# Performance work log

Measured on AMD Instinct MI355X. Metric: run time of the kernel, lower is better.

## Reference

```python
import jax, jax.numpy as jnp
import numpy as np

N_NODES = 50000
N_EDGES = 800000
IN_CH = 128
HID_CH = 128
OUT_CH = 64
K = 25
LRELU_SLOPE = 0.01  # torch.nn.LeakyReLU default
NORM_EPS = 1e-12    # F.normalize default eps


def setup_inputs() -> dict:
    key = jax.random.key(0)
    ks = jax.random.split(key, 8)
    x = jax.random.normal(ks[0], (N_NODES, IN_CH), dtype=jnp.float32)
    edge_index = jax.random.randint(ks[1], (2, N_EDGES), 0, N_NODES, dtype=jnp.int32)
    # ChebConv per-order weights [K, in, hid] + bias
    W = jax.random.normal(ks[2], (K, IN_CH, HID_CH), dtype=jnp.float32) / np.sqrt(IN_CH)
    b = jax.random.normal(ks[3], (HID_CH,), dtype=jnp.float32) * 0.01
    # mu / logstd linear heads
    w_mu = jax.random.normal(ks[4], (HID_CH, OUT_CH), dtype=jnp.float32) / np.sqrt(HID_CH)
    b_mu = jax.random.normal(ks[5], (OUT_CH,), dtype=jnp.float32) * 0.01
    w_ls = jax.random.normal(ks[6], (HID_CH, OUT_CH), dtype=jnp.float32) / np.sqrt(HID_CH)
    b_ls = jax.random.normal(ks[7], (OUT_CH,), dtype=jnp.float32) * 0.01
    return {"x": x, "edge_index": edge_index, "W": W, "b": b,
            "w_mu": w_mu, "b_mu": b_mu, "w_ls": w_ls, "b_ls": b_ls}


def _cheb_conv(x, edge_index, W, b):
    # PyG ChebConv with normalization='sym', lambda_max=2.0:
    # scaled Laplacian L~ = L - I = -D^{-1/2} A D^{-1/2} (diagonal nets to zero)
    src, dst = edge_index[0], edge_index[1]
    deg = jax.ops.segment_sum(jnp.ones(src.shape[0], x.dtype), src, num_segments=x.shape[0])
    dis = jnp.where(deg > 0, jax.lax.rsqrt(jnp.where(deg > 0, deg, 1.0)), 0.0)
    enorm = -dis[src] * dis[dst]  # [E]

    def prop(h):  # out[i] = sum_{(j->i)} enorm_e * h[j]
        return jax.ops.segment_sum(enorm[:, None] * h[src], dst, num_segments=h.shape[0])

    tx0 = x
    tx1 = prop(x)
    out0 = tx0 @ W[0] + tx1 @ W[1]

    def step(carry, Wk):
        t1, t0, acc = carry
        t2 = 2.0 * prop(t1) - t0  # Chebyshev recurrence
        return (t2, t1, acc + t2 @ Wk), None

    (_, _, out), _ = jax.lax.scan(step, (tx1, tx0, out0), W[2:])
    return out + b


def reference(x, edge_index, W, b, w_mu, b_mu, w_ls, b_ls):
    h = _cheb_conv(x, edge_index, W, b)
    # eval mode: dropout is identity
    h = jnp.where(h > 0, h, LRELU_SLOPE * h)
    mu = h @ w_mu + b_mu
    ls = h @ w_ls + b_ls
    nrm = jnp.sqrt(jnp.sum(ls * ls, axis=1, keepdims=True))
    logstd = ls / jnp.maximum(nrm, NORM_EPS) * 1.8
    zeta = mu  # eval-mode reparam returns mu
    return (mu, logstd, zeta)
```

## Files before the change

### kernel.cpp

```cpp
#include <hip/hip_runtime.h>
#include <hip/hip_fp16.h>

#define N_NODES 50000
#define N_EDGES 800000
#define CH 128
#define OUT_CH 64
#define K_ORD 25
#define SLICE ((size_t)N_NODES * CH)

typedef __attribute__((ext_vector_type(8))) short s16x8;
typedef __attribute__((ext_vector_type(4))) float f32x4;

union U4H8 { uint4 u; __half2 h2[4]; ushort us[8]; };

__global__ void count_kernel(const int* __restrict__ ei, float* __restrict__ deg,
                             int* __restrict__ indeg, int E) {
    int e = blockIdx.x * blockDim.x + threadIdx.x;
    if (e >= E) return;
    int s = ei[e];
    int d = ei[E + e];
    atomicAdd(&deg[s], 1.0f);
    atomicAdd(&indeg[d], 1);
}

__global__ __launch_bounds__(256) void scan1_kernel(const int* __restrict__ indeg,
                                                    int* __restrict__ loc,
                                                    int* __restrict__ bsum, int n) {
    __shared__ int tmp[256];
    int tid = threadIdx.x;
    int i = blockIdx.x * 256 + tid;
    int v = (i < n) ? indeg[i] : 0;
    tmp[tid] = v;
    __syncthreads();
    for (int off = 1; off < 256; off <<= 1) {
        int t = (tid >= off) ? tmp[tid - off] : 0;
        __syncthreads();
        tmp[tid] += t;
        __syncthreads();
    }
    if (i < n) loc[i] = tmp[tid] - v;
    if (tid == 255) bsum[blockIdx.x] = tmp[255];
}

__global__ __launch_bounds__(256) void scan2_kernel(int* __restrict__ bsum, int nb) {
    __shared__ int tmp[256];
    int tid = threadIdx.x;
    int v = (tid < nb) ? bsum[tid] : 0;
    tmp[tid] = v;
    __syncthreads();
    for (int off = 1; off < 256; off <<= 1) {
        int t = (tid >= off) ? tmp[tid - off] : 0;
        __syncthreads();
        tmp[tid] += t;
        __syncthreads();
    }
    if (tid < nb) bsum[tid] = tmp[tid] - v;
    if (tid == 255) bsum[nb] = tmp[255];
}

__global__ __launch_bounds__(256) void scan3_kernel(const int* __restrict__ loc,
                                                    const int* __restrict__ bsum,
                                                    int* __restrict__ rowptr,
                                                    int* __restrict__ cursor, int n, int nb) {
    int i = blockIdx.x * 256 + threadIdx.x;
    if (i < n) {
        int r = loc[i] + bsum[i >> 8];
        rowptr[i] = r;
        cursor[i] = r;
    }
    if (i == n) rowptr[n] = bsum[nb];
}

__global__ void scatter_kernel(const int* __restrict__ ei, const float* __restrict__ deg,
                               int* __restrict__ cursor, int* __restrict__ col,
                               float* __restrict__ ew, int E) {
    int e = blockIdx.x * blockDim.x + threadIdx.x;
    if (e >= E) return;
    int s = ei[e];
    int d = ei[E + e];
    float ds = deg[s], dd = deg[d];
    float dis_s = ds > 0.f ? rsqrtf(ds) : 0.f;
    float dis_d = dd > 0.f ? rsqrtf(dd) : 0.f;
    int pos = atomicAdd(&cursor[d], 1);
    col[pos] = s;
    ew[pos] = -dis_s * dis_d;
}

__global__ __launch_bounds__(256) void cvt_kernel(const float* __restrict__ in,
                                                  ushort* __restrict__ out, int n8) {
    int i = blockIdx.x * 256 + threadIdx.x;
    if (i >= n8) return;
    float4 a = ((const float4*)in)[2 * i];
    float4 b = ((const float4*)in)[2 * i + 1];
    U4H8 p;
    p.h2[0] = __float22half2_rn(make_float2(a.x, a.y));
    p.h2[1] = __float22half2_rn(make_float2(a.z, a.w));
    p.h2[2] = __float22half2_rn(make_float2(b.x, b.y));
    p.h2[3] = __float22half2_rn(make_float2(b.z, b.w));
    ((uint4*)out)[i] = p.u;
}

__global__ __launch_bounds__(256) void wprep_kernel(const float* __restrict__ W,
                                                    ushort* __restrict__ WT) {
    int idx = blockIdx.x * 256 + threadIdx.x;
    if (idx >= K_ORD * 128 * 32) return;
    int c4 = idx & 31;
    int nrow = (idx >> 5) & 127;
    int k = idx >> 12;
    const float* Wk = W + (size_t)k * CH * CH;
    ushort o[4];
    #pragma unroll
    for (int j = 0; j < 4; ++j)
        o[j] = __half_as_ushort(__float2half_rn(Wk[(c4 * 4 + j) * CH + nrow]));
    *(ushort2*)(WT + (size_t)k * CH * CH + nrow * CH + c4 * 4)     = make_ushort2(o[0], o[1]);
    *(ushort2*)(WT + (size_t)k * CH * CH + nrow * CH + c4 * 4 + 2) = make_ushort2(o[2], o[3]);
}

__global__ __launch_bounds__(256) void prop_kernel(
    const ushort* __restrict__ tin, const ushort* __restrict__ tprev,
    ushort* __restrict__ tout, const int* __restrict__ rowptr,
    const int* __restrict__ col, const float* __restrict__ ew, int n, int mode) {
    int wid = blockIdx.x * 4 + (threadIdx.x >> 6);
    if (wid >= n) return;
    int lane = threadIdx.x & 63;
    int g = lane >> 4, sub = lane & 15;
    int beg = rowptr[wid], end = rowptr[wid + 1];
    float acc[8] = {0.f, 0.f, 0.f, 0.f, 0.f, 0.f, 0.f, 0.f};
    for (int e0 = beg; e0 < end; e0 += 64) {
        int ne = min(64, end - e0);
        int c = 0; float w = 0.f;
        if (lane < ne) { c = col[e0 + lane]; w = ew[e0 + lane]; }
        for (int j4 = 0; j4 < ne; j4 += 4) {
            int j = j4 + g;
            int cj = __shfl(c, j & 63);
            float wj = __shfl(w, j & 63);
            if (j >= ne) wj = 0.f;
            U4H8 v;
            v.u = ((const uint4*)(tin + (size_t)cj * CH))[sub];
            #pragma unroll
            for (int t = 0; t < 4; ++t) {
                float2 f = __half22float2(v.h2[t]);
                acc[2 * t]     = fmaf(wj, f.x, acc[2 * t]);
                acc[2 * t + 1] = fmaf(wj, f.y, acc[2 * t + 1]);
            }
        }
    }
    #pragma unroll
    for (int i = 0; i < 8; ++i) {
        acc[i] += __shfl_xor(acc[i], 16);
        acc[i] += __shfl_xor(acc[i], 32);
    }
    if (g == 0) {
        size_t base = (size_t)wid * CH + sub * 8;
        float r[8];
        if (mode) {
            U4H8 pv;
            pv.u = *(const uint4*)(tprev + base);
            #pragma unroll
            for (int t = 0; t < 4; ++t) {
                float2 f = __half22float2(pv.h2[t]);
                r[2 * t]     = 2.f * acc[2 * t]     - f.x;
                r[2 * t + 1] = 2.f * acc[2 * t + 1] - f.y;
            }
        } else {
            #pragma unroll
            for (int i = 0; i < 8; ++i) r[i] = acc[i];
        }
        U4H8 p;
        p.h2[0] = __float22half2_rn(make_float2(r[0], r[1]));
        p.h2[1] = __float22half2_rn(make_float2(r[2], r[3]));
        p.h2[2] = __float22half2_rn(make_float2(r[4], r[5]));
        p.h2[3] = __float22half2_rn(make_float2(r[6], r[7]));
        *(uint4*)(tout + base) = p.u;
    }
}

__global__ __launch_bounds__(256) void gemm_kernel(
    const ushort* __restrict__ T, size_t slice_stride, const ushort* __restrict__ WT,
    float* __restrict__ C, int M, int k0, int nk, int beta) {
    __shared__ ushort As[128 * 128];
    __shared__ ushort Ws[128 * 128];
    int tid = threadIdx.x;
    int row0 = blockIdx.x * 128;
    int wave = tid >> 6, lane = tid & 63;
    int wrow = wave * 32;
    int lr = lane & 15, kg = lane >> 4;

    f32x4 acc[2][8];
    #pragma unroll
    for (int a = 0; a < 2; ++a)
        #pragma unroll
        for (int c = 0; c < 8; ++c)
            acc[a][c] = (f32x4){0.f, 0.f, 0.f, 0.f};

    for (int ks = 0; ks < nk; ++ks) {
        const ushort* Ak = T + (size_t)(k0 + ks) * slice_stride;
        const ushort* Wk = WT + (size_t)(k0 + ks) * (CH * CH);
        #pragma unroll
        for (int i = 0; i < 8; ++i) {
            int idx = tid + i * 256;
            int r = idx >> 4, gg = idx & 15;
            uint4 v = make_uint4(0u, 0u, 0u, 0u);
            int gr = row0 + r;
            if (gr < M) v = ((const uint4*)(Ak + (size_t)gr * CH))[gg];
            int gs = gg ^ (r & 15);
            *(uint4*)(&As[r * 128 + gs * 8]) = v;
        }
        #pragma unroll
        for (int i = 0; i < 8; ++i) {
            int idx = tid + i * 256;
            int r = idx >> 4, gg = idx & 15;
            uint4 v = ((const uint4*)(Wk + (size_t)r * CH))[gg];
            int gs = gg ^ (r & 15);
            *(uint4*)(&Ws[r * 128 + gs * 8]) = v;
        }
        __syncthreads();

        #pragma unroll
        for (int kc = 0; kc < 4; ++kc) {
            int gbase = kc * 4 + kg;
            int gs = gbase ^ lr;
            s16x8 a0 = *(const s16x8*)(&As[(wrow + lr) * 128 + gs * 8]);
            s16x8 a1 = *(const s16x8*)(&As[(wrow + 16 + lr) * 128 + gs * 8]);
            #pragma unroll
            for (int c = 0; c < 8; ++c) {
                s16x8 bfr = *(const s16x8*)(&Ws[(c * 16 + lr) * 128 + gs * 8]);
                acc[0][c] = __builtin_amdgcn_mfma_f32_16x16x32_f16(a0, bfr, acc[0][c], 0, 0, 0);
                acc[1][c] = __builtin_amdgcn_mfma_f32_16x16x32_f16(a1, bfr, acc[1][c], 0, 0, 0);
            }
        }
        __syncthreads();
    }

    #pragma unroll
    for (int rf = 0; rf < 2; ++rf)
        #pragma unroll
        for (int c = 0; c < 8; ++c)
            #pragma unroll
            for (int j = 0; j < 4; ++j) {
                int gr = row0 + wrow + rf * 16 + kg * 4 + j;
                int gc = c * 16 + lr;
                if (gr < M) {
                    float v = acc[rf][c][j];
                    if (beta) v += C[(size_t)gr * 128 + gc];
                    C[(size_t)gr * 128 + gc] = v;
                }
            }
}

__global__ __launch_bounds__(256) void head_kernel(
    const float* __restrict__ acc_in, const float* __restrict__ b,
    const float* __restrict__ w_mu, const float* __restrict__ b_mu,
    const float* __restrict__ w_ls, const float* __restrict__ b_ls,
    float* __restrict__ out, int M) {
    __shared__ ushort Hs[128 * 128];
    __shared__ ushort Ws[128 * 128];
    __shared__ float s_b[128];
    int tid = threadIdx.x;
    int row0 = blockIdx.x * 128;
    if (tid < 128) s_b[tid] = b[tid];
    __syncthreads();

    #pragma unroll
    for (int i = 0; i < 16; ++i) {
        int idx = tid + i * 256;
        int r = idx >> 5, c4 = idx & 31;
        float4 v = make_float4(0.f, 0.f, 0.f, 0.f);
        int gr = row0 + r;
        if (gr < M) v = ((const float4*)(acc_in + (size_t)gr * CH))[c4];
        float hv[4] = { v.x, v.y, v.z, v.w };
        #pragma unroll
        for (int j = 0; j < 4; ++j) {
            float h = hv[j] + s_b[c4 * 4 + j];
            hv[j] = h > 0.f ? h : 0.01f * h;
        }
        __half2 p0 = __float22half2_rn(make_float2(hv[0], hv[1]));
        __half2 p1 = __float22half2_rn(make_float2(hv[2], hv[3]));
        int gg = c4 >> 1, hh = c4 & 1;
        int gs = gg ^ (r & 15);
        uint2 pk;
        pk.x = *(unsigned int*)&p0;
        pk.y = *(unsigned int*)&p1;
        *(uint2*)(&Hs[r * 128 + gs * 8 + hh * 4]) = pk;
    }
    #pragma unroll
    for (int i = 0; i < 16; ++i) {
        int idx = tid + i * 256;
        int k = idx >> 5, n4 = idx & 31;
        const float* src = (n4 < 16) ? w_mu : w_ls;
        float4 v = ((const float4*)src)[k * 16 + (n4 & 15)];
        int gk = k >> 3, kk = k & 7;
        float vv[4] = { v.x, v.y, v.z, v.w };
        #pragma unroll
        for (int j = 0; j < 4; ++j) {
            int nn = n4 * 4 + j;
            int gs = gk ^ (nn & 15);
            Ws[nn * 128 + gs * 8 + kk] = __half_as_ushort(__float2half_rn(vv[j]));
        }
    }
    __syncthreads();

    int wave = tid >> 6, lane = tid & 63;
    int wrow = wave * 32;
    int lr = lane & 15, kg = lane >> 4;
    f32x4 acc[2][8];
    #pragma unroll
    for (int a = 0; a < 2; ++a)
        #pragma unroll
        for (int c = 0; c < 8; ++c)
            acc[a][c] = (f32x4){0.f, 0.f, 0.f, 0.f};

    #pragma unroll
    for (int kc = 0; kc < 4; ++kc) {
        int gbase = kc * 4 + kg;
        int gs = gbase ^ lr;
        s16x8 a0 = *(const s16x8*)(&Hs[(wrow + lr) * 128 + gs * 8]);
        s16x8 a1 = *(const s16x8*)(&Hs[(wrow + 16 + lr) * 128 + gs * 8]);
        #pragma unroll
        for (int c = 0; c < 8; ++c) {
            s16x8 bfr = *(const s16x8*)(&Ws[(c * 16 + lr) * 128 + gs * 8]);
            acc[0][c] = __builtin_amdgcn_mfma_f32_16x16x32_f16(a0, bfr, acc[0][c], 0, 0, 0);
            acc[1][c] = __builtin_amdgcn_mfma_f32_16x16x32_f16(a1, bfr, acc[1][c], 0, 0, 0);
        }
    }

    #pragma unroll
    for (int rf = 0; rf < 2; ++rf)
        #pragma unroll
        for (int j = 0; j < 4; ++j) {
            int gr = row0 + wrow + rf * 16 + kg * 4 + j;
            float muv[4], lsv[4];
            float s2 = 0.f;
            #pragma unroll
            for (int c = 0; c < 4; ++c) {
                muv[c] = acc[rf][c][j] + b_mu[c * 16 + lr];
                float l = acc[rf][4 + c][j] + b_ls[c * 16 + lr];
                lsv[c] = l;
                s2 = fmaf(l, l, s2);
            }
            s2 += __shfl_xor(s2, 1);
            s2 += __shfl_xor(s2, 2);
            s2 += __shfl_xor(s2, 4);
            s2 += __shfl_xor(s2, 8);
            float sc = 1.8f / fmaxf(sqrtf(s2), 1e-12f);
            if (gr < M) {
                size_t base = (size_t)gr * OUT_CH;
                #pragma unroll
                for (int c = 0; c < 4; ++c) {
                    int gc = c * 16 + lr;
                    out[base + gc] = muv[c];
                    out[(size_t)N_NODES * OUT_CH + base + gc] = lsv[c] * sc;
                    out[2 * (size_t)N_NODES * OUT_CH + base + gc] = muv[c];
                }
            }
        }
}

extern "C" void kernel_launch(void* const* d_in, const int* in_sizes, int n_in,
                              void* d_out, int out_size, void* d_ws, size_t ws_size,
                              hipStream_t stream) {
    const float* x    = (const float*)d_in[0];
    const int*   ei   = (const int*)d_in[1];
    const float* W    = (const float*)d_in[2];
    const float* b    = (const float*)d_in[3];
    const float* w_mu = (const float*)d_in[4];
    const float* b_mu = (const float*)d_in[5];
    const float* w_ls = (const float*)d_in[6];
    const float* b_ls = (const float*)d_in[7];

    const int N = N_NODES, E = N_EDGES;
    const int NB = (N + 255) / 256;
    char* p = (char*)d_ws;
    auto alloc = [&](size_t bytes) {
        char* r = p;
        p += (bytes + 511) & ~(size_t)511;
        return r;
    };
    float*  deg    = (float*)alloc((size_t)N * 4);
    int*    indeg  = (int*)alloc((size_t)N * 4);
    int*    rowptr = (int*)alloc((size_t)(N + 1) * 4);
    int*    cursor = (int*)alloc((size_t)N * 4);
    int*    loc    = (int*)alloc((size_t)N * 4);
    int*    bsum   = (int*)alloc((size_t)(NB + 1) * 4);
    int*    col    = (int*)alloc((size_t)E * 4);
    float*  ew     = (float*)alloc((size_t)E * 4);
    ushort* WT     = (ushort*)alloc((size_t)K_ORD * CH * CH * 2);
    float*  accbuf = (float*)alloc((size_t)N * CH * 4);

    size_t used_common = (size_t)(p - (char*)d_ws);
    size_t tbuf_bytes  = (size_t)K_ORD * SLICE * 2;
    bool bigpath = ws_size >= used_common + tbuf_bytes + (1u << 20);

    hipMemsetAsync(deg, 0, (size_t)N * 4, stream);
    hipMemsetAsync(indeg, 0, (size_t)N * 4, stream);

    count_kernel<<<(E + 255) / 256, 256, 0, stream>>>(ei, deg, indeg, E);
    scan1_kernel<<<NB, 256, 0, stream>>>(indeg, loc, bsum, N);
    scan2_kernel<<<1, 256, 0, stream>>>(bsum, NB);
    scan3_kernel<<<NB, 256, 0, stream>>>(loc, bsum, rowptr, cursor, N, NB);
    scatter_kernel<<<(E + 255) / 256, 256, 0, stream>>>(ei, deg, cursor, col, ew, E);
    wprep_kernel<<<(K_ORD * 128 * 32 + 255) / 256, 256, 0, stream>>>(W, WT);

    int gemm_grid = (N + 127) / 128;
    int prop_grid = (N + 3) / 4;

    if (bigpath) {
        ushort* Tbuf = (ushort*)alloc(tbuf_bytes);
        cvt_kernel<<<(N * CH / 8 + 255) / 256, 256, 0, stream>>>(x, Tbuf, N * CH / 8);
        prop_kernel<<<prop_grid, 256, 0, stream>>>(Tbuf, Tbuf, Tbuf + SLICE,
                                                   rowptr, col, ew, N, 0);
        for (int k = 2; k < K_ORD; ++k)
            prop_kernel<<<prop_grid, 256, 0, stream>>>(
                Tbuf + (size_t)(k - 1) * SLICE, Tbuf + (size_t)(k - 2) * SLICE,
                Tbuf + (size_t)k * SLICE, rowptr, col, ew, N, 1);
        gemm_kernel<<<gemm_grid, 256, 0, stream>>>(Tbuf, SLICE, WT, accbuf, N, 0, K_ORD, 0);
    } else {
        ushort* r0 = (ushort*)alloc(SLICE * 2);
        ushort* r1 = (ushort*)alloc(SLICE * 2);
        ushort* r2 = (ushort*)alloc(SLICE * 2);
        cvt_kernel<<<(N * CH / 8 + 255) / 256, 256, 0, stream>>>(x, r0, N * CH / 8);
        gemm_kernel<<<gemm_grid, 256, 0, stream>>>(r0, 0, WT, accbuf, N, 0, 1, 0);
        prop_kernel<<<prop_grid, 256, 0, stream>>>(r0, r0, r1, rowptr, col, ew, N, 0);
        gemm_kernel<<<gemm_grid, 256, 0, stream>>>(r1, 0, WT, accbuf, N, 1, 1, 1);
        ushort* tm2 = r0;
        ushort* tm1 = r1;
        ushort* tnx = r2;
        for (int k = 2; k < K_ORD; ++k) {
            prop_kernel<<<prop_grid, 256, 0, stream>>>(tm1, tm2, tnx, rowptr, col, ew, N, 1);
            gemm_kernel<<<gemm_grid, 256, 0, stream>>>(tnx, 0, WT, accbuf, N, k, 1, 1);
            ushort* t = tm2; tm2 = tm1; tm1 = tnx; tnx = t;
        }
    }

    head_kernel<<<gemm_grid, 256, 0, stream>>>(accbuf, b, w_mu, b_mu, w_ls, b_ls,
                                               (float*)d_out, N);
}
```

Measured before the change: 1.577 ms.

## Split feature channels into two 64-wide halves for cache-resident propagation

```diff
diff --git a/kernel.cpp b/kernel.cpp
--- a/kernel.cpp
+++ b/kernel.cpp
@@ -7,11 +7,13 @@
 #define OUT_CH 64
 #define K_ORD 25
 #define SLICE ((size_t)N_NODES * CH)
+#define HS ((size_t)N_NODES * 64)
 
 typedef __attribute__((ext_vector_type(8))) short s16x8;
 typedef __attribute__((ext_vector_type(4))) float f32x4;
-
-union U4H8 { uint4 u; __half2 h2[4]; ushort us[8]; };
+typedef __attribute__((ext_vector_type(4))) unsigned int u32x4;
+
+union U4H8 { uint4 u; u32x4 v4; __half2 h2[4]; ushort us[8]; };
 
 __global__ void count_kernel(const int* __restrict__ ei, float* __restrict__ deg,
                              int* __restrict__ indeg, int E) {
@@ -87,9 +89,11 @@
 }
 
 __global__ __launch_bounds__(256) void cvt_kernel(const float* __restrict__ in,
-                                                  ushort* __restrict__ out, int n8) {
+                                                  ushort* __restrict__ T0, int ng) {
     int i = blockIdx.x * 256 + threadIdx.x;
-    if (i >= n8) return;
+    if (i >= ng) return;
+    int r = i >> 4, gg = i & 15;
+    int h = gg >> 3, sub = gg & 7;
     float4 a = ((const float4*)in)[2 * i];
     float4 b = ((const float4*)in)[2 * i + 1];
     U4H8 p;
@@ -97,7 +101,7 @@
     p.h2[1] = __float22half2_rn(make_float2(a.z, a.w));
     p.h2[2] = __float22half2_rn(make_float2(b.x, b.y));
     p.h2[3] = __float22half2_rn(make_float2(b.z, b.w));
-    ((uint4*)out)[i] = p.u;
+    ((uint4*)(T0 + (size_t)h * HS))[(size_t)r * 8 + sub] = p.u;
 }
 
 __global__ __launch_bounds__(256) void wprep_kernel(const float* __restrict__ W,
@@ -123,20 +127,23 @@
     int wid = blockIdx.x * 4 + (threadIdx.x >> 6);
     if (wid >= n) return;
     int lane = threadIdx.x & 63;
-    int g = lane >> 4, sub = lane & 15;
+    int g = lane >> 3, sub = lane & 7;
     int beg = rowptr[wid], end = rowptr[wid + 1];
     float acc[8] = {0.f, 0.f, 0.f, 0.f, 0.f, 0.f, 0.f, 0.f};
     for (int e0 = beg; e0 < end; e0 += 64) {
         int ne = min(64, end - e0);
         int c = 0; float w = 0.f;
-        if (lane < ne) { c = col[e0 + lane]; w = ew[e0 + lane]; }
-        for (int j4 = 0; j4 < ne; j4 += 4) {
-            int j = j4 + g;
+        if (lane < ne) {
+            c = __builtin_nontemporal_load(col + e0 + lane);
+            w = __builtin_nontemporal_load(ew + e0 + lane);
+        }
+        for (int j8 = 0; j8 < ne; j8 += 8) {
+            int j = j8 + g;
             int cj = __shfl(c, j & 63);
             float wj = __shfl(w, j & 63);
             if (j >= ne) wj = 0.f;
             U4H8 v;
-            v.u = ((const uint4*)(tin + (size_t)cj * CH))[sub];
+            v.u = ((const uint4*)(tin + (size_t)cj * 64))[sub];
             #pragma unroll
             for (int t = 0; t < 4; ++t) {
                 float2 f = __half22float2(v.h2[t]);
@@ -147,15 +154,16 @@
     }
     #pragma unroll
     for (int i = 0; i < 8; ++i) {
+        acc[i] += __shfl_xor(acc[i], 8);
         acc[i] += __shfl_xor(acc[i], 16);
         acc[i] += __shfl_xor(acc[i], 32);
     }
     if (g == 0) {
-        size_t base = (size_t)wid * CH + sub * 8;
+        size_t base = (size_t)wid * 64 + sub * 8;
         float r[8];
         if (mode) {
             U4H8 pv;
-            pv.u = *(const uint4*)(tprev + base);
+            pv.v4 = __builtin_nontemporal_load((const u32x4*)(tprev + base));
             #pragma unroll
             for (int t = 0; t < 4; ++t) {
                 float2 f = __half22float2(pv.h2[t]);
@@ -171,13 +179,13 @@
         p.h2[1] = __float22half2_rn(make_float2(r[2], r[3]));
         p.h2[2] = __float22half2_rn(make_float2(r[4], r[5]));
         p.h2[3] = __float22half2_rn(make_float2(r[6], r[7]));
-        *(uint4*)(tout + base) = p.u;
+        __builtin_nontemporal_store(p.v4, (u32x4*)(tout + base));
     }
 }
 
 __global__ __launch_bounds__(256) void gemm_kernel(
-    const ushort* __restrict__ T, size_t slice_stride, const ushort* __restrict__ WT,
-    float* __restrict__ C, int M, int k0, int nk, int beta) {
+    const ushort* __restrict__ T, size_t kstride, const ushort* __restrict__ WT,
+    float* __restrict__ C, int M, int wk0, int nk, int beta) {
     __shared__ ushort As[128 * 128];
     __shared__ ushort Ws[128 * 128];
     int tid = threadIdx.x;
@@ -194,15 +202,16 @@
             acc[a][c] = (f32x4){0.f, 0.f, 0.f, 0.f};
 
     for (int ks = 0; ks < nk; ++ks) {
-        const ushort* Ak = T + (size_t)(k0 + ks) * slice_stride;
-        const ushort* Wk = WT + (size_t)(k0 + ks) * (CH * CH);
+        const ushort* Ak = T + (size_t)ks * kstride;
+        const ushort* Wk = WT + (size_t)(wk0 + ks) * (CH * CH);
         #pragma unroll
         for (int i = 0; i < 8; ++i) {
             int idx = tid + i * 256;
             int r = idx >> 4, gg = idx & 15;
+            int h = gg >> 3, sub = gg & 7;
             uint4 v = make_uint4(0u, 0u, 0u, 0u);
             int gr = row0 + r;
-            if (gr < M) v = ((const uint4*)(Ak + (size_t)gr * CH))[gg];
+            if (gr < M) v = ((const uint4*)(Ak + (size_t)h * HS + (size_t)gr * 64))[sub];
             int gs = gg ^ (r & 15);
             *(uint4*)(&As[r * 128 + gs * 8]) = v;
         }
@@ -387,9 +396,8 @@
     ushort* WT     = (ushort*)alloc((size_t)K_ORD * CH * CH * 2);
     float*  accbuf = (float*)alloc((size_t)N * CH * 4);
 
-    size_t used_common = (size_t)(p - (char*)d_ws);
-    size_t tbuf_bytes  = (size_t)K_ORD * SLICE * 2;
-    bool bigpath = ws_size >= used_common + tbuf_bytes + (1u << 20);
+    size_t used = (size_t)(p - (char*)d_ws);
+    bool bigpath = ws_size >= used + (size_t)K_ORD * SLICE * 2 + (1u << 20);
 
     hipMemsetAsync(deg, 0, (size_t)N * 4, stream);
     hipMemsetAsync(indeg, 0, (size_t)N * 4, stream);
@@ -403,32 +411,40 @@
 
     int gemm_grid = (N + 127) / 128;
     int prop_grid = (N + 3) / 4;
+    int cvt_grid = (N * 16 + 255) / 256;
 
     if (bigpath) {
-        ushort* Tbuf = (ushort*)alloc(tbuf_bytes);
-        cvt_kernel<<<(N * CH / 8 + 255) / 256, 256, 0, stream>>>(x, Tbuf, N * CH / 8);
-        prop_kernel<<<prop_grid, 256, 0, stream>>>(Tbuf, Tbuf, Tbuf + SLICE,
-                                                   rowptr, col, ew, N, 0);
-        for (int k = 2; k < K_ORD; ++k)
-            prop_kernel<<<prop_grid, 256, 0, stream>>>(
-                Tbuf + (size_t)(k - 1) * SLICE, Tbuf + (size_t)(k - 2) * SLICE,
-                Tbuf + (size_t)k * SLICE, rowptr, col, ew, N, 1);
-        gemm_kernel<<<gemm_grid, 256, 0, stream>>>(Tbuf, SLICE, WT, accbuf, N, 0, K_ORD, 0);
+        ushort* T = (ushort*)alloc((size_t)K_ORD * SLICE * 2);
+        cvt_kernel<<<cvt_grid, 256, 0, stream>>>(x, T, N * 16);
+        for (int h = 0; h < 2; ++h) {
+            ushort* Th = T + (size_t)h * HS;
+            prop_kernel<<<prop_grid, 256, 0, stream>>>(Th, Th, Th + 2 * HS,
+                                                       rowptr, col, ew, N, 0);
+            for (int k = 2; k < K_ORD; ++k)
+                prop_kernel<<<prop_grid, 256, 0, stream>>>(
+                    Th + (size_t)(k - 1) * 2 * HS, Th + (size_t)(k - 2) * 2 * HS,
+                    Th + (size_t)k * 2 * HS, rowptr, col, ew, N, 1);
+        }
+        gemm_kernel<<<gemm_grid, 256, 0, stream>>>(T, 2 * HS, WT, accbuf, N, 0, K_ORD, 0);
     } else {
         ushort* r0 = (ushort*)alloc(SLICE * 2);
         ushort* r1 = (ushort*)alloc(SLICE * 2);
         ushort* r2 = (ushort*)alloc(SLICE * 2);
-        cvt_kernel<<<(N * CH / 8 + 255) / 256, 256, 0, stream>>>(x, r0, N * CH / 8);
+        ushort* Ss[3] = { r0, r1, r2 };
+        cvt_kernel<<<cvt_grid, 256, 0, stream>>>(x, r0, N * 16);
         gemm_kernel<<<gemm_grid, 256, 0, stream>>>(r0, 0, WT, accbuf, N, 0, 1, 0);
-        prop_kernel<<<prop_grid, 256, 0, stream>>>(r0, r0, r1, rowptr, col, ew, N, 0);
+        for (int h = 0; h < 2; ++h)
+            prop_kernel<<<prop_grid, 256, 0, stream>>>(r0 + (size_t)h * HS,
+                                                       r0 + (size_t)h * HS,
+                                                       r1 + (size_t)h * HS,
+                                                       rowptr, col, ew, N, 0);
         gemm_kernel<<<gemm_grid, 256, 0, stream>>>(r1, 0, WT, accbuf, N, 1, 1, 1);
-        ushort* tm2 = r0;
-        ushort* tm1 = r1;
-        ushort* tnx = r2;
         for (int k = 2; k < K_ORD; ++k) {
-            prop_kernel<<<prop_grid, 256, 0, stream>>>(tm1, tm2, tnx, rowptr, col, ew, N, 1);
-            gemm_kernel<<<gemm_grid, 256, 0, stream>>>(tnx, 0, WT, accbuf, N, k, 1, 1);
-            ushort* t = tm2; tm2 = tm1; tm1 = tnx; tnx = t;
+            for (int h = 0; h < 2; ++h)
+                prop_kernel<<<prop_grid, 256, 0, stream>>>(
+                    Ss[(k - 1) % 3] + (size_t)h * HS, Ss[(k - 2) % 3] + (size_t)h * HS,
+                    Ss[k % 3] + (size_t)h * HS, rowptr, col, ew, N, 1);
+            gemm_kernel<<<gemm_grid, 256, 0, stream>>>(Ss[k % 3], 0, WT, accbuf, N, k, 1, 1);
         }
     }
 
```

Result: slower. 2.063 ms (+30.8%).

## Rescale Chebyshev basis to drop edge weights and partition gathers by source range

Applied to the files above, without the earlier changes.

```diff
diff --git a/kernel.cpp b/kernel.cpp
--- a/kernel.cpp
+++ b/kernel.cpp
@@ -7,20 +7,24 @@
 #define OUT_CH 64
 #define K_ORD 25
 #define SLICE ((size_t)N_NODES * CH)
+#define RANGES 4
+#define RSZ 12500
+#define NODES_PB 49
+#define N4 (N_NODES * RANGES)
 
 typedef __attribute__((ext_vector_type(8))) short s16x8;
 typedef __attribute__((ext_vector_type(4))) float f32x4;
 
 union U4H8 { uint4 u; __half2 h2[4]; ushort us[8]; };
 
-__global__ void count_kernel(const int* __restrict__ ei, float* __restrict__ deg,
-                             int* __restrict__ indeg, int E) {
+__global__ void count_kernel(const int* __restrict__ ei, int* __restrict__ deg_i,
+                             int* __restrict__ indeg4, int E) {
     int e = blockIdx.x * blockDim.x + threadIdx.x;
     if (e >= E) return;
     int s = ei[e];
     int d = ei[E + e];
-    atomicAdd(&deg[s], 1.0f);
-    atomicAdd(&indeg[d], 1);
+    atomicAdd(&deg_i[s], 1);
+    atomicAdd(&indeg4[d * RANGES + (s / RSZ)], 1);
 }
 
 __global__ __launch_bounds__(256) void scan1_kernel(const int* __restrict__ indeg,
@@ -42,61 +46,79 @@
     if (tid == 255) bsum[blockIdx.x] = tmp[255];
 }
 
-__global__ __launch_bounds__(256) void scan2_kernel(int* __restrict__ bsum, int nb) {
-    __shared__ int tmp[256];
+__global__ __launch_bounds__(1024) void scan2_kernel(int* __restrict__ bsum, int nb) {
+    __shared__ int tmp[1024];
     int tid = threadIdx.x;
     int v = (tid < nb) ? bsum[tid] : 0;
     tmp[tid] = v;
     __syncthreads();
-    for (int off = 1; off < 256; off <<= 1) {
+    for (int off = 1; off < 1024; off <<= 1) {
         int t = (tid >= off) ? tmp[tid - off] : 0;
         __syncthreads();
         tmp[tid] += t;
         __syncthreads();
     }
     if (tid < nb) bsum[tid] = tmp[tid] - v;
-    if (tid == 255) bsum[nb] = tmp[255];
+    if (tid == 1023) bsum[nb] = tmp[1023];
 }
 
 __global__ __launch_bounds__(256) void scan3_kernel(const int* __restrict__ loc,
                                                     const int* __restrict__ bsum,
                                                     int* __restrict__ rowptr,
-                                                    int* __restrict__ cursor, int n, int nb) {
+                                                    int* __restrict__ cursor, int n) {
     int i = blockIdx.x * 256 + threadIdx.x;
     if (i < n) {
         int r = loc[i] + bsum[i >> 8];
         rowptr[i] = r;
         cursor[i] = r;
     }
-    if (i == n) rowptr[n] = bsum[nb];
-}
-
-__global__ void scatter_kernel(const int* __restrict__ ei, const float* __restrict__ deg,
-                               int* __restrict__ cursor, int* __restrict__ col,
-                               float* __restrict__ ew, int E) {
+    if (i == n) rowptr[n] = bsum[(n + 255) >> 8];
+}
+
+__global__ void scatter_kernel(const int* __restrict__ ei, int* __restrict__ cursor,
+                               int* __restrict__ col, int E) {
     int e = blockIdx.x * blockDim.x + threadIdx.x;
     if (e >= E) return;
     int s = ei[e];
     int d = ei[E + e];
-    float ds = deg[s], dd = deg[d];
-    float dis_s = ds > 0.f ? rsqrtf(ds) : 0.f;
-    float dis_d = dd > 0.f ? rsqrtf(dd) : 0.f;
-    int pos = atomicAdd(&cursor[d], 1);
+    int r = s / RSZ;
+    int pos = atomicAdd(&cursor[d * RANGES + r], 1);
     col[pos] = s;
-    ew[pos] = -dis_s * dis_d;
+}
+
+__global__ __launch_bounds__(256) void scaleprep_kernel(const int* __restrict__ deg_i,
+                                                        float* __restrict__ beta,
+                                                        float* __restrict__ alpha,
+                                                        float* __restrict__ gam, int n) {
+    int i = blockIdx.x * 256 + threadIdx.x;
+    if (i >= n) return;
+    int dg = deg_i[i];
+    if (dg > 0) {
+        float fd = (float)dg;
+        beta[i] = -2.f / fd;
+        alpha[i] = rsqrtf(fd);
+        gam[i] = sqrtf(fd);
+    } else {
+        beta[i] = 0.f;
+        alpha[i] = 1.f;
+        gam[i] = 1.f;
+    }
 }
 
 __global__ __launch_bounds__(256) void cvt_kernel(const float* __restrict__ in,
+                                                  const float* __restrict__ alpha,
                                                   ushort* __restrict__ out, int n8) {
     int i = blockIdx.x * 256 + threadIdx.x;
     if (i >= n8) return;
+    int row = i >> 4;
+    float al = alpha[row];
     float4 a = ((const float4*)in)[2 * i];
     float4 b = ((const float4*)in)[2 * i + 1];
     U4H8 p;
-    p.h2[0] = __float22half2_rn(make_float2(a.x, a.y));
-    p.h2[1] = __float22half2_rn(make_float2(a.z, a.w));
-    p.h2[2] = __float22half2_rn(make_float2(b.x, b.y));
-    p.h2[3] = __float22half2_rn(make_float2(b.z, b.w));
+    p.h2[0] = __float22half2_rn(make_float2(al * a.x, al * a.y));
+    p.h2[1] = __float22half2_rn(make_float2(al * a.z, al * a.w));
+    p.h2[2] = __float22half2_rn(make_float2(al * b.x, al * b.y));
+    p.h2[3] = __float22half2_rn(make_float2(al * b.z, al * b.w));
     ((uint4*)out)[i] = p.u;
 }
 
@@ -118,66 +140,90 @@
 
 __global__ __launch_bounds__(256) void prop_kernel(
     const ushort* __restrict__ tin, const ushort* __restrict__ tprev,
-    ushort* __restrict__ tout, const int* __restrict__ rowptr,
-    const int* __restrict__ col, const float* __restrict__ ew, int n, int mode) {
-    int wid = blockIdx.x * 4 + (threadIdx.x >> 6);
-    if (wid >= n) return;
-    int lane = threadIdx.x & 63;
+    ushort* __restrict__ tout, const int* __restrict__ rowptr4,
+    const int* __restrict__ col, const float* __restrict__ beta,
+    int n, int mode) {
+    __shared__ float accs[NODES_PB * 128];
+    int tid = threadIdx.x;
+    for (int i = tid; i < NODES_PB * 128; i += 256) accs[i] = 0.f;
+    __syncthreads();
+    int wv = tid >> 6, lane = tid & 63;
     int g = lane >> 4, sub = lane & 15;
-    int beg = rowptr[wid], end = rowptr[wid + 1];
-    float acc[8] = {0.f, 0.f, 0.f, 0.f, 0.f, 0.f, 0.f, 0.f};
-    for (int e0 = beg; e0 < end; e0 += 64) {
-        int ne = min(64, end - e0);
-        int c = 0; float w = 0.f;
-        if (lane < ne) { c = col[e0 + lane]; w = ew[e0 + lane]; }
-        for (int j4 = 0; j4 < ne; j4 += 4) {
-            int j = j4 + g;
-            int cj = __shfl(c, j & 63);
-            float wj = __shfl(w, j & 63);
-            if (j >= ne) wj = 0.f;
-            U4H8 v;
-            v.u = ((const uint4*)(tin + (size_t)cj * CH))[sub];
+    int nbase = blockIdx.x * NODES_PB;
+
+    for (int r = 0; r < RANGES; ++r) {
+        for (int ln = wv; ln < NODES_PB; ln += 4) {
+            int nid = nbase + ln;
+            if (nid >= n) break;
+            int beg = rowptr4[nid * RANGES + r];
+            int end = rowptr4[nid * RANGES + r + 1];
+            if (beg == end) continue;
+            float acc[8] = {0.f, 0.f, 0.f, 0.f, 0.f, 0.f, 0.f, 0.f};
+            for (int e0 = beg; e0 < end; e0 += 64) {
+                int ne = min(64, end - e0);
+                int c = 0;
+                if (lane < ne) c = col[e0 + lane];
+                for (int j4 = 0; j4 < ne; j4 += 4) {
+                    int j = j4 + g;
+                    int cj = __shfl(c, j & 63);
+                    float m = (j < ne) ? 1.f : 0.f;
+                    U4H8 v;
+                    v.u = ((const uint4*)(tin + (size_t)cj * CH))[sub];
+                    #pragma unroll
+                    for (int t = 0; t < 4; ++t) {
+                        float2 f = __half22float2(v.h2[t]);
+                        acc[2 * t]     = fmaf(m, f.x, acc[2 * t]);
+                        acc[2 * t + 1] = fmaf(m, f.y, acc[2 * t + 1]);
+                    }
+                }
+            }
             #pragma unroll
-            for (int t = 0; t < 4; ++t) {
-                float2 f = __half22float2(v.h2[t]);
-                acc[2 * t]     = fmaf(wj, f.x, acc[2 * t]);
-                acc[2 * t + 1] = fmaf(wj, f.y, acc[2 * t + 1]);
-            }
-        }
-    }
-    #pragma unroll
-    for (int i = 0; i < 8; ++i) {
-        acc[i] += __shfl_xor(acc[i], 16);
-        acc[i] += __shfl_xor(acc[i], 32);
-    }
-    if (g == 0) {
-        size_t base = (size_t)wid * CH + sub * 8;
-        float r[8];
-        if (mode) {
-            U4H8 pv;
-            pv.u = *(const uint4*)(tprev + base);
-            #pragma unroll
-            for (int t = 0; t < 4; ++t) {
-                float2 f = __half22float2(pv.h2[t]);
-                r[2 * t]     = 2.f * acc[2 * t]     - f.x;
-                r[2 * t + 1] = 2.f * acc[2 * t + 1] - f.y;
-            }
-        } else {
-            #pragma unroll
-            for (int i = 0; i < 8; ++i) r[i] = acc[i];
-        }
-        U4H8 p;
-        p.h2[0] = __float22half2_rn(make_float2(r[0], r[1]));
-        p.h2[1] = __float22half2_rn(make_float2(r[2], r[3]));
-        p.h2[2] = __float22half2_rn(make_float2(r[4], r[5]));
-        p.h2[3] = __float22half2_rn(make_float2(r[6], r[7]));
-        *(uint4*)(tout + base) = p.u;
+            for (int i = 0; i < 8; ++i) {
+                acc[i] += __shfl_xor(acc[i], 16);
+                acc[i] += __shfl_xor(acc[i], 32);
+            }
+            if (g == 0) {
+                float* row = &accs[ln * 128 + sub * 8];
+                #pragma unroll
+                for (int i = 0; i < 8; ++i) row[i] += acc[i];
+            }
+        }
+    }
+    for (int ln = wv; ln < NODES_PB; ln += 4) {
+        int nid = nbase + ln;
+        if (nid >= n) break;
+        if (g == 0) {
+            float bt = beta[nid];
+            const float* row = &accs[ln * 128 + sub * 8];
+            size_t base = (size_t)nid * CH + sub * 8;
+            float rr[8];
+            if (mode) {
+                U4H8 pv;
+                pv.u = *(const uint4*)(tprev + base);
+                #pragma unroll
+                for (int t = 0; t < 4; ++t) {
+                    float2 f = __half22float2(pv.h2[t]);
+                    rr[2 * t]     = fmaf(bt, row[2 * t],     -f.x);
+                    rr[2 * t + 1] = fmaf(bt, row[2 * t + 1], -f.y);
+                }
+            } else {
+                #pragma unroll
+                for (int i = 0; i < 8; ++i) rr[i] = 0.5f * bt * row[i];
+            }
+            U4H8 p;
+            p.h2[0] = __float22half2_rn(make_float2(rr[0], rr[1]));
+            p.h2[1] = __float22half2_rn(make_float2(rr[2], rr[3]));
+            p.h2[2] = __float22half2_rn(make_float2(rr[4], rr[5]));
+            p.h2[3] = __float22half2_rn(make_float2(rr[6], rr[7]));
+            *(uint4*)(tout + base) = p.u;
+        }
     }
 }
 
 __global__ __launch_bounds__(256) void gemm_kernel(
-    const ushort* __restrict__ T, size_t slice_stride, const ushort* __restrict__ WT,
-    float* __restrict__ C, int M, int k0, int nk, int beta) {
+    const ushort* __restrict__ T, size_t kstride, const ushort* __restrict__ WT,
+    const float* __restrict__ gam, float* __restrict__ C,
+    int M, int wk0, int nk, int betaf) {
     __shared__ ushort As[128 * 128];
     __shared__ ushort Ws[128 * 128];
     int tid = threadIdx.x;
@@ -194,17 +240,26 @@
             acc[a][c] = (f32x4){0.f, 0.f, 0.f, 0.f};
 
     for (int ks = 0; ks < nk; ++ks) {
-        const ushort* Ak = T + (size_t)(k0 + ks) * slice_stride;
-        const ushort* Wk = WT + (size_t)(k0 + ks) * (CH * CH);
+        const ushort* Ak = T + (size_t)ks * kstride;
+        const ushort* Wk = WT + (size_t)(wk0 + ks) * (CH * CH);
         #pragma unroll
         for (int i = 0; i < 8; ++i) {
             int idx = tid + i * 256;
             int r = idx >> 4, gg = idx & 15;
-            uint4 v = make_uint4(0u, 0u, 0u, 0u);
             int gr = row0 + r;
-            if (gr < M) v = ((const uint4*)(Ak + (size_t)gr * CH))[gg];
+            U4H8 hv;
+            hv.u = make_uint4(0u, 0u, 0u, 0u);
+            if (gr < M) {
+                hv.u = ((const uint4*)(Ak + (size_t)gr * CH))[gg];
+                float gm = gam[gr];
+                #pragma unroll
+                for (int t = 0; t < 4; ++t) {
+                    float2 f = __half22float2(hv.h2[t]);
+                    hv.h2[t] = __float22half2_rn(make_float2(gm * f.x, gm * f.y));
+                }
+            }
             int gs = gg ^ (r & 15);
-            *(uint4*)(&As[r * 128 + gs * 8]) = v;
+            *(uint4*)(&As[r * 128 + gs * 8]) = hv.u;
         }
         #pragma unroll
         for (int i = 0; i < 8; ++i) {
@@ -242,7 +297,7 @@
                 int gc = c * 16 + lr;
                 if (gr < M) {
                     float v = acc[rf][c][j];
-                    if (beta) v += C[(size_t)gr * 128 + gc];
+                    if (betaf) v += C[(size_t)gr * 128 + gc];
                     C[(size_t)gr * 128 + gc] = v;
                 }
             }
@@ -369,66 +424,69 @@
     const float* b_ls = (const float*)d_in[7];
 
     const int N = N_NODES, E = N_EDGES;
-    const int NB = (N + 255) / 256;
+    const int NB4 = (N4 + 255) / 256;
     char* p = (char*)d_ws;
     auto alloc = [&](size_t bytes) {
         char* r = p;
         p += (bytes + 511) & ~(size_t)511;
         return r;
     };
-    float*  deg    = (float*)alloc((size_t)N * 4);
-    int*    indeg  = (int*)alloc((size_t)N * 4);
-    int*    rowptr = (int*)alloc((size_t)(N + 1) * 4);
-    int*    cursor = (int*)alloc((size_t)N * 4);
-    int*    loc    = (int*)alloc((size_t)N * 4);
-    int*    bsum   = (int*)alloc((size_t)(NB + 1) * 4);
-    int*    col    = (int*)alloc((size_t)E * 4);
-    float*  ew     = (float*)alloc((size_t)E * 4);
-    ushort* WT     = (ushort*)alloc((size_t)K_ORD * CH * CH * 2);
-    float*  accbuf = (float*)alloc((size_t)N * CH * 4);
-
-    size_t used_common = (size_t)(p - (char*)d_ws);
-    size_t tbuf_bytes  = (size_t)K_ORD * SLICE * 2;
-    bool bigpath = ws_size >= used_common + tbuf_bytes + (1u << 20);
-
-    hipMemsetAsync(deg, 0, (size_t)N * 4, stream);
-    hipMemsetAsync(indeg, 0, (size_t)N * 4, stream);
-
-    count_kernel<<<(E + 255) / 256, 256, 0, stream>>>(ei, deg, indeg, E);
-    scan1_kernel<<<NB, 256, 0, stream>>>(indeg, loc, bsum, N);
-    scan2_kernel<<<1, 256, 0, stream>>>(bsum, NB);
-    scan3_kernel<<<NB, 256, 0, stream>>>(loc, bsum, rowptr, cursor, N, NB);
-    scatter_kernel<<<(E + 255) / 256, 256, 0, stream>>>(ei, deg, cursor, col, ew, E);
+    int*    deg_i   = (int*)alloc((size_t)N * 4);
+    int*    indeg4  = (int*)alloc((size_t)N4 * 4);
+    int*    rowptr4 = (int*)alloc((size_t)(N4 + 1) * 4);
+    int*    cursor4 = (int*)alloc((size_t)N4 * 4);
+    int*    loc     = (int*)alloc((size_t)N4 * 4);
+    int*    bsum    = (int*)alloc((size_t)(NB4 + 1) * 4);
+    int*    col     = (int*)alloc((size_t)E * 4);
+    float*  beta    = (float*)alloc((size_t)N * 4);
+    float*  alpha   = (float*)alloc((size_t)N * 4);
+    float*  gam     = (float*)alloc((size_t)N * 4);
+    ushort* WT      = (ushort*)alloc((size_t)K_ORD * CH * CH * 2);
+    float*  accbuf  = (float*)alloc((size_t)N * CH * 4);
+
+    size_t used = (size_t)(p - (char*)d_ws);
+    bool bigpath = ws_size >= used + (size_t)K_ORD * SLICE * 2 + (1u << 20);
+
+    hipMemsetAsync(deg_i, 0, (size_t)N * 4, stream);
+    hipMemsetAsync(indeg4, 0, (size_t)N4 * 4, stream);
+
+    count_kernel<<<(E + 255) / 256, 256, 0, stream>>>(ei, deg_i, indeg4, E);
+    scan1_kernel<<<NB4, 256, 0, stream>>>(indeg4, loc, bsum, N4);
+    scan2_kernel<<<1, 1024, 0, stream>>>(bsum, NB4);
+    scan3_kernel<<<(N4 + 256) / 256, 256, 0, stream>>>(loc, bsum, rowptr4, cursor4, N4);
+    scatter_kernel<<<(E + 255) / 256, 256, 0, stream>>>(ei, cursor4, col, E);
+    scaleprep_kernel<<<(N + 255) / 256, 256, 0, stream>>>(deg_i, beta, alpha, gam, N);
     wprep_kernel<<<(K_ORD * 128 * 32 + 255) / 256, 256, 0, stream>>>(W, WT);
 
     int gemm_grid = (N + 127) / 128;
-    int prop_grid = (N + 3) / 4;
+    int prop_grid = (N + NODES_PB - 1) / NODES_PB;
+    int cvt_grid = (N * 16 + 255) / 256;
 
     if (bigpath) {
-        ushort* Tbuf = (ushort*)alloc(tbuf_bytes);
-        cvt_kernel<<<(N * CH / 8 + 255) / 256, 256, 0, stream>>>(x, Tbuf, N * CH / 8);
-        prop_kernel<<<prop_grid, 256, 0, stream>>>(Tbuf, Tbuf, Tbuf + SLICE,
-                                                   rowptr, col, ew, N, 0);
+        ushort* T = (ushort*)alloc((size_t)K_ORD * SLICE * 2);
+        cvt_kernel<<<cvt_grid, 256, 0, stream>>>(x, alpha, T, N * 16);
+        prop_kernel<<<prop_grid, 256, 0, stream>>>(T, T, T + SLICE,
+                                                   rowptr4, col, beta, N, 0);
         for (int k = 2; k < K_ORD; ++k)
             prop_kernel<<<prop_grid, 256, 0, stream>>>(
-                Tbuf + (size_t)(k - 1) * SLICE, Tbuf + (size_t)(k - 2) * SLICE,
-                Tbuf + (size_t)k * SLICE, rowptr, col, ew, N, 1);
-        gemm_kernel<<<gemm_grid, 256, 0, stream>>>(Tbuf, SLICE, WT, accbuf, N, 0, K_ORD, 0);
+                T + (size_t)(k - 1) * SLICE, T + (size_t)(k - 2) * SLICE,
+                T + (size_t)k * SLICE, rowptr4, col, beta, N, 1);
+        gemm_kernel<<<gemm_grid, 256, 0, stream>>>(T, SLICE, WT, gam, accbuf,
+                                                   N, 0, K_ORD, 0);
     } else {
         ushort* r0 = (ushort*)alloc(SLICE * 2);
         ushort* r1 = (ushort*)alloc(SLICE * 2);
         ushort* r2 = (ushort*)alloc(SLICE * 2);
-        cvt_kernel<<<(N * CH / 8 + 255) / 256, 256, 0, stream>>>(x, r0, N * CH / 8);
-        gemm_kernel<<<gemm_grid, 256, 0, stream>>>(r0, 0, WT, accbuf, N, 0, 1, 0);
-        prop_kernel<<<prop_grid, 256, 0, stream>>>(r0, r0, r1, rowptr, col, ew, N, 0);
-        gemm_kernel<<<gemm_grid, 256, 0, stream>>>(r1, 0, WT, accbuf, N, 1, 1, 1);
-        ushort* tm2 = r0;
-        ushort* tm1 = r1;
-        ushort* tnx = r2;
+        ushort* Ss[3] = { r0, r1, r2 };
+        cvt_kernel<<<cvt_grid, 256, 0, stream>>>(x, alpha, r0, N * 16);
+        gemm_kernel<<<gemm_grid, 256, 0, stream>>>(r0, 0, WT, gam, accbuf, N, 0, 1, 0);
+        prop_kernel<<<prop_grid, 256, 0, stream>>>(r0, r0, r1, rowptr4, col, beta, N, 0);
+        gemm_kernel<<<gemm_grid, 256, 0, stream>>>(r1, 0, WT, gam, accbuf, N, 1, 1, 1);
         for (int k = 2; k < K_ORD; ++k) {
-            prop_kernel<<<prop_grid, 256, 0, stream>>>(tm1, tm2, tnx, rowptr, col, ew, N, 1);
-            gemm_kernel<<<gemm_grid, 256, 0, stream>>>(tnx, 0, WT, accbuf, N, k, 1, 1);
-            ushort* t = tm2; tm2 = tm1; tm1 = tnx; tnx = t;
+            prop_kernel<<<prop_grid, 256, 0, stream>>>(
+                Ss[(k - 1) % 3], Ss[(k - 2) % 3], Ss[k % 3], rowptr4, col, beta, N, 1);
+            gemm_kernel<<<gemm_grid, 256, 0, stream>>>(Ss[k % 3], 0, WT, gam, accbuf,
+                                                       N, k, 1, 1);
         }
     }
 
```

After: 2.987 ms. 1.89x slower.
